# Kernel tuning notes

Hardware: AMD Instinct MI355X
Metric: run time of the kernel (lower is better)

Reference implementation:

```python
import jax, jax.numpy as jnp
import numpy as np

N_NODES = 50000
N_EDGES = 1000000
IN_DIM, HID_DIM, OUT_DIM = 128, 64, 16


def setup_inputs() -> dict:
    key = jax.random.key(0)
    k1, k2, k3, k4 = jax.random.split(key, 4)
    x = jax.random.normal(k1, (N_NODES, IN_DIM), dtype=jnp.float32)
    edge_index = jax.random.randint(k2, (2, N_EDGES), 0, N_NODES, dtype=jnp.int64)
    # Glorot-style scaling for weights, zero bias (PyG GCNConv default init style)
    W1 = jax.random.normal(k3, (IN_DIM, HID_DIM), dtype=jnp.float32) * (1.0 / np.sqrt(IN_DIM))
    b1 = jnp.zeros((HID_DIM,), dtype=jnp.float32)
    W2 = jax.random.normal(k4, (HID_DIM, OUT_DIM), dtype=jnp.float32) * (1.0 / np.sqrt(HID_DIM))
    b2 = jnp.zeros((OUT_DIM,), dtype=jnp.float32)
    return {"x": x, "edge_index": edge_index, "W1": W1, "b1": b1, "W2": W2, "b2": b2}


def gcn_conv(x, src, dst, W, b, num_nodes):
    """PyG GCNConv: add self loops, symmetric deg^{-1/2} normalization,
    linear transform, gather-scale-scatter aggregation, bias."""
    # degree includes self loops (src/dst already augmented by caller)
    deg = jax.ops.segment_sum(jnp.ones_like(dst, dtype=x.dtype), dst, num_segments=num_nodes)
    dinv = jnp.where(deg > 0, deg ** -0.5, 0.0)
    norm = dinv[src] * dinv[dst]            # [E']
    h = x @ W                                # [N, F_out] transform before aggregation
    msg = h[src] * norm[:, None]             # gather + scale
    out = jax.ops.segment_sum(msg, dst, num_segments=num_nodes)  # scatter-add
    return out + b


def reference(x, edge_index, W1, b1, W2, b2):
    n = x.shape[0]
    loops = jnp.arange(n, dtype=edge_index.dtype)
    src = jnp.concatenate([edge_index[0], loops])
    dst = jnp.concatenate([edge_index[1], loops])
    h = gcn_conv(x, src, dst, W1, b1, n)
    h = jax.nn.relu(h)
    out = gcn_conv(h, src, dst, W2, b2, n)
    return out
```

## Files before the change

kernel.cpp:

```cpp
#include <hip/hip_runtime.h>

#define IN_DIM 128
#define HID_DIM 64
#define OUT_DIM 16

#define SSHIFT 7
#define SMASK 127
#define CHUNK 4096
#define CBLK 1024
#define KPT (CHUNK / CBLK)
#define CAP 4096

#define G1S 132

#define SW_OFF   0
#define SX_OFF   32768
#define SDV_OFF  66560
#define SMEM_BYTES 67072

static __device__ __forceinline__ unsigned short f2bf(float f) {
    unsigned u = __float_as_uint(f);
    unsigned r = u + 0x7fffu + ((u >> 16) & 1u);
    return (unsigned short)(r >> 16);
}
static __device__ __forceinline__ unsigned packbf2(float a, float b) {
    return (unsigned)f2bf(a) | ((unsigned)f2bf(b) << 16);
}
static __device__ __forceinline__ float bflo(unsigned v) { return __uint_as_float(v << 16); }
static __device__ __forceinline__ float bfhi(unsigned v) { return __uint_as_float(v & 0xffff0000u); }

__global__ __launch_bounds__(CBLK) void passC2(const int* __restrict__ src,
                                               const int* __restrict__ dst,
                                               int* __restrict__ gcnt,
                                               int* __restrict__ eb,
                                               int E, int NS) {
    __shared__ int cnt[512];
    __shared__ int lofs[512];
    __shared__ int bofs[512];
    __shared__ int cur[512];
    __shared__ int srt[CHUNK];
    int t = threadIdx.x;
    if (t < 512) cnt[t] = 0;
    __syncthreads();
    int base = blockIdx.x * CHUNK;
    int dreg[KPT];
    #pragma unroll
    for (int k = 0; k < KPT; ++k) {
        int i = base + k * CBLK + t;
        int d = -1;
        if (i < E) { d = dst[i]; atomicAdd(&cnt[d >> SSHIFT], 1); }
        dreg[k] = d;
    }
    __syncthreads();
    if (t < 512) lofs[t] = cnt[t];
    __syncthreads();
    for (int off = 1; off < 512; off <<= 1) {
        int tmp = 0;
        if (t < 512 && t >= off) tmp = lofs[t - off];
        __syncthreads();
        if (t < 512) lofs[t] += tmp;
        __syncthreads();
    }
    if (t < 512) {
        int c  = cnt[t];
        int lo = lofs[t] - c;
        lofs[t] = lo;
        cur[t]  = lo;
        bofs[t] = (t < NS && c) ? atomicAdd(&gcnt[t], c) : 0;
    }
    __syncthreads();
    #pragma unroll
    for (int k = 0; k < KPT; ++k) {
        int i = base + k * CBLK + t;
        if (i < E) {
            int d = dreg[k];
            int s = d >> SSHIFT;
            int p = atomicAdd(&cur[s], 1);
            srt[p] = src[i] | ((d & SMASK) << 17);
        }
    }
    __syncthreads();
    int wave = t >> 6, lane = t & 63;
    for (int s = wave; s < NS; s += CBLK / 64) {
        int c  = cnt[s];
        int lo = lofs[s];
        size_t gb = (size_t)s * CAP + bofs[s];
        for (int k = lane; k < c; k += 64) eb[gb + k] = srt[lo + k];
    }
}

__global__ __launch_bounds__(256) void passDG(const int* __restrict__ eb,
                                              const int* __restrict__ tot,
                                              const float* __restrict__ x,
                                              const float* __restrict__ W1,
                                              int* __restrict__ csr_src,
                                              int* __restrict__ row_ptr,
                                              float* __restrict__ dinv,
                                              unsigned* __restrict__ h1u,
                                              int N, int E, int NS) {
    __shared__ __align__(16) char smem[SMEM_BYTES];
    int s = blockIdx.x, t = threadIdx.x;

    {
        int* red  = (int*)smem;
        int* deg  = red + 256;
        int* incl = deg + 128;
        int* cur  = incl + 128;
        int* srt  = cur + 128;
        float* sdv = (float*)(smem + SDV_OFF);

        if (t < 128) deg[t] = 0;
        int part = 0;
        for (int k = t; k < s; k += 256) part += tot[k];
        red[t] = part;
        __syncthreads();
        for (int off = 128; off >= 1; off >>= 1) {
            if (t < off) red[t] += red[t + off];
            __syncthreads();
        }
        int b0 = red[0];
        int cnt = tot[s];
        const size_t sbase = (size_t)s * CAP;
        for (int k = t; k < cnt; k += 256) atomicAdd(&deg[eb[sbase + k] >> 17], 1);
        __syncthreads();
        if (t < 128) incl[t] = deg[t];
        __syncthreads();
        for (int off = 1; off < 128; off <<= 1) {
            int tmp = 0;
            if (t < 128 && t >= off) tmp = incl[t - off];
            __syncthreads();
            if (t < 128) incl[t] += tmp;
            __syncthreads();
        }
        if (t < 128) {
            int loff = incl[t] - deg[t];
            cur[t] = loff;
            float dn = rsqrtf((float)(deg[t] + 1));
            sdv[t] = dn;
            int n = (s << SSHIFT) + t;
            if (n < N) {
                row_ptr[n] = b0 + loff;
                dinv[n] = dn;
            }
        }
        if (s == NS - 1 && t == 0) row_ptr[N] = E;
        __syncthreads();
        for (int k = t; k < cnt; k += 256) {
            int v = eb[sbase + k];
            int dl = v >> 17;
            int p = atomicAdd(&cur[dl], 1);
            srt[p] = v & 0x1FFFF;
        }
        __syncthreads();
        for (int k = t; k < cnt; k += 256) csr_src[b0 + k] = srt[k];
    }
    __syncthreads();

    {
        float* sW  = (float*)(smem + SW_OFF);
        float* sx  = (float*)(smem + SX_OFF);
        float* sdv = (float*)(smem + SDV_OFF);

        const float4* W4  = (const float4*)W1;
        float4*       sW4 = (float4*)sW;
        #pragma unroll
        for (int i = 0; i < 8; ++i) sW4[i * 256 + t] = W4[i * 256 + t];

        const float4* x4 = (const float4*)x;
        int og = t & 15, ng = t >> 4;

        for (int st = 0; st < 2; ++st) {
            int node0 = (s << SSHIFT) + st * 64;
            __syncthreads();
            for (int i = t; i < 64 * 32; i += 256) {
                int r = i >> 5, c = i & 31;
                int n = node0 + r; if (n >= N) n = 0;
                *(float4*)(sx + r * G1S + c * 4) = x4[(size_t)n * 32 + c];
            }
            __syncthreads();

            float a00=0.f,a01=0.f,a02=0.f,a03=0.f, a10=0.f,a11=0.f,a12=0.f,a13=0.f,
                  a20=0.f,a21=0.f,a22=0.f,a23=0.f, a30=0.f,a31=0.f,a32=0.f,a33=0.f;
            const float* xr = sx + (ng << 2) * G1S;
            #pragma unroll 4
            for (int k = 0; k < IN_DIM; ++k) {
                float x0 = xr[k];
                float x1 = xr[G1S + k];
                float x2 = xr[2 * G1S + k];
                float x3 = xr[3 * G1S + k];
                float4 wv = ((const float4*)(sW + k * HID_DIM))[og];
                a00 = fmaf(x0, wv.x, a00); a01 = fmaf(x0, wv.y, a01);
                a02 = fmaf(x0, wv.z, a02); a03 = fmaf(x0, wv.w, a03);
                a10 = fmaf(x1, wv.x, a10); a11 = fmaf(x1, wv.y, a11);
                a12 = fmaf(x1, wv.z, a12); a13 = fmaf(x1, wv.w, a13);
                a20 = fmaf(x2, wv.x, a20); a21 = fmaf(x2, wv.y, a21);
                a22 = fmaf(x2, wv.z, a22); a23 = fmaf(x2, wv.w, a23);
                a30 = fmaf(x3, wv.x, a30); a31 = fmaf(x3, wv.y, a31);
                a32 = fmaf(x3, wv.z, a32); a33 = fmaf(x3, wv.w, a33);
            }

            int lb = st * 64 + (ng << 2);
            int nb = (s << SSHIFT) + st * 64 + (ng << 2);
#define G1_STORE(i, c0, c1, c2, c3)                                         \
            {                                                               \
                int n = nb + i;                                             \
                if (n < N) {                                                \
                    float dn = sdv[lb + i];                                 \
                    uint2 pv;                                               \
                    pv.x = packbf2(c0 * dn, c1 * dn);                       \
                    pv.y = packbf2(c2 * dn, c3 * dn);                       \
                    ((uint2*)(h1u + (size_t)n * 32))[og] = pv;              \
                }                                                           \
            }
            G1_STORE(0, a00, a01, a02, a03)
            G1_STORE(1, a10, a11, a12, a13)
            G1_STORE(2, a20, a21, a22, a23)
            G1_STORE(3, a30, a31, a32, a33)
#undef G1_STORE
        }

        if (s == NS - 1 && t < 16) {
            uint2 z; z.x = 0u; z.y = 0u;
            ((uint2*)(h1u + (size_t)N * 32))[t] = z;
        }
    }
}

__global__ __launch_bounds__(256) void agg1_kernel(const unsigned* __restrict__ h1u,
                                                   const int* __restrict__ row_ptr,
                                                   const int* __restrict__ csr_src,
                                                   const float* __restrict__ dinv,
                                                   const float* __restrict__ b1,
                                                   const float* __restrict__ W2,
                                                   unsigned* __restrict__ h2u, int N) {
    __shared__ __align__(16) float sW[OUT_DIM * 68];
    int t = threadIdx.x;
    for (int i = t; i < HID_DIM * OUT_DIM; i += 256) {
        int k = i >> 4, j = i & 15;
        sW[j * 68 + k] = W2[i];
    }
    __syncthreads();

    int lane = t & 63;
    int h  = lane >> 5;
    int l  = lane & 31;
    int es = l >> 3;
    int dg = l & 7;
    int n = blockIdx.x * 8 + ((t >> 6) << 1) + h;
    if (n > N) return;
    if (n == N) {
        if (l < 4) { uint2 z; z.x = 0u; z.y = 0u; ((uint2*)h2u)[(size_t)N * 4 + l] = z; }
        return;
    }

    int e0 = row_ptr[n], e1 = row_ptr[n + 1];
    const uint4* rb = (const uint4*)h1u;
    int sb = h << 5;

    float a0 = 0.f, a1 = 0.f, a2 = 0.f, a3 = 0.f,
          a4 = 0.f, a5 = 0.f, a6 = 0.f, a7 = 0.f;

    for (int base = e0 - 1; base < e1; base += 32) {
        int idx = base + l;
        int sld = N;
        if (idx == e0 - 1) sld = n;
        else if (idx < e1) sld = csr_src[idx];
        int lim = e1 - base;
        if (lim > 32) lim = 32;
        int nr = (lim + 3) >> 2;
        nr = (nr + 1) & ~1;
        for (int r = 0; r < nr; r += 2) {
            int sA = __shfl(sld, sb + ((r + 0) << 2) + es);
            int sB = __shfl(sld, sb + ((r + 1) << 2) + es);
            uint4 vA = rb[(size_t)sA * 8 + dg];
            uint4 vB = rb[(size_t)sB * 8 + dg];
            a0 += bflo(vA.x) + bflo(vB.x);
            a1 += bfhi(vA.x) + bfhi(vB.x);
            a2 += bflo(vA.y) + bflo(vB.y);
            a3 += bfhi(vA.y) + bfhi(vB.y);
            a4 += bflo(vA.z) + bflo(vB.z);
            a5 += bfhi(vA.z) + bfhi(vB.z);
            a6 += bflo(vA.w) + bflo(vB.w);
            a7 += bfhi(vA.w) + bfhi(vB.w);
        }
    }
    #pragma unroll
    for (int m = 8; m <= 16; m <<= 1) {
        a0 += __shfl_xor(a0, m); a1 += __shfl_xor(a1, m);
        a2 += __shfl_xor(a2, m); a3 += __shfl_xor(a3, m);
        a4 += __shfl_xor(a4, m); a5 += __shfl_xor(a5, m);
        a6 += __shfl_xor(a6, m); a7 += __shfl_xor(a7, m);
    }

    float dn = dinv[n];
    float4 bA = ((const float4*)b1)[2 * dg];
    float4 bB = ((const float4*)b1)[2 * dg + 1];
    float r0 = fmaxf(fmaf(dn, a0, bA.x), 0.f);
    float r1 = fmaxf(fmaf(dn, a1, bA.y), 0.f);
    float r2 = fmaxf(fmaf(dn, a2, bA.z), 0.f);
    float r3 = fmaxf(fmaf(dn, a3, bA.w), 0.f);
    float r4 = fmaxf(fmaf(dn, a4, bB.x), 0.f);
    float r5 = fmaxf(fmaf(dn, a5, bB.y), 0.f);
    float r6 = fmaxf(fmaf(dn, a6, bB.z), 0.f);
    float r7 = fmaxf(fmaf(dn, a7, bB.w), 0.f);

    const float* wb = sW + ((es << 2) * 68) + (dg << 3);
    float4 wA, wB2;
    wA = *(const float4*)(wb);        wB2 = *(const float4*)(wb + 4);
    float p0 = r0*wA.x + r1*wA.y + r2*wA.z + r3*wA.w + r4*wB2.x + r5*wB2.y + r6*wB2.z + r7*wB2.w;
    wA = *(const float4*)(wb + 68);   wB2 = *(const float4*)(wb + 72);
    float p1 = r0*wA.x + r1*wA.y + r2*wA.z + r3*wA.w + r4*wB2.x + r5*wB2.y + r6*wB2.z + r7*wB2.w;
    wA = *(const float4*)(wb + 136);  wB2 = *(const float4*)(wb + 140);
    float p2 = r0*wA.x + r1*wA.y + r2*wA.z + r3*wA.w + r4*wB2.x + r5*wB2.y + r6*wB2.z + r7*wB2.w;
    wA = *(const float4*)(wb + 204);  wB2 = *(const float4*)(wb + 208);
    float p3 = r0*wA.x + r1*wA.y + r2*wA.z + r3*wA.w + r4*wB2.x + r5*wB2.y + r6*wB2.z + r7*wB2.w;

    #pragma unroll
    for (int m = 1; m <= 4; m <<= 1) {
        p0 += __shfl_xor(p0, m); p1 += __shfl_xor(p1, m);
        p2 += __shfl_xor(p2, m); p3 += __shfl_xor(p3, m);
    }
    if (dg == 0) {
        uint2 pv;
        pv.x = packbf2(p0 * dn, p1 * dn);
        pv.y = packbf2(p2 * dn, p3 * dn);
        ((uint2*)h2u)[(size_t)n * 4 + es] = pv;
    }
}

__global__ __launch_bounds__(256) void agg2_kernel(const unsigned* __restrict__ h2u,
                                                   const int* __restrict__ row_ptr,
                                                   const int* __restrict__ csr_src,
                                                   const float* __restrict__ dinv,
                                                   const float* __restrict__ b2,
                                                   float* __restrict__ out, int N) {
    int t = threadIdx.x;
    int lane = t & 63;
    int h  = lane >> 4;
    int l  = lane & 15;
    int es = l >> 2;
    int dg = l & 3;
    int n = blockIdx.x * 16 + ((t >> 6) << 2) + h;
    if (n >= N) return;

    int e0 = row_ptr[n], e1 = row_ptr[n + 1];
    const uint2* rb = (const uint2*)h2u;
    int sb = h << 4;

    float a0 = 0.f, a1 = 0.f, a2 = 0.f, a3 = 0.f;

    for (int base = e0 - 1; base < e1; base += 16) {
        int idx = base + l;
        int sld = N;
        if (idx == e0 - 1) sld = n;
        else if (idx < e1) sld = csr_src[idx];
        int lim = e1 - base;
        if (lim > 16) lim = 16;
        int nr = (lim + 3) >> 2;
        nr = (nr + 1) & ~1;
        for (int r = 0; r < nr; r += 2) {
            int sA = __shfl(sld, sb + ((r + 0) << 2) + es);
            int sB = __shfl(sld, sb + ((r + 1) << 2) + es);
            uint2 vA = rb[(size_t)sA * 4 + dg];
            uint2 vB = rb[(size_t)sB * 4 + dg];
            a0 += bflo(vA.x) + bflo(vB.x);
            a1 += bfhi(vA.x) + bfhi(vB.x);
            a2 += bflo(vA.y) + bflo(vB.y);
            a3 += bfhi(vA.y) + bfhi(vB.y);
        }
    }
    #pragma unroll
    for (int m = 4; m <= 8; m <<= 1) {
        a0 += __shfl_xor(a0, m); a1 += __shfl_xor(a1, m);
        a2 += __shfl_xor(a2, m); a3 += __shfl_xor(a3, m);
    }
    if (es == 0) {
        float dn = dinv[n];
        float4 bb = ((const float4*)b2)[dg];
        float4 r;
        r.x = fmaf(dn, a0, bb.x);
        r.y = fmaf(dn, a1, bb.y);
        r.z = fmaf(dn, a2, bb.z);
        r.w = fmaf(dn, a3, bb.w);
        ((float4*)out)[(size_t)n * 4 + dg] = r;
    }
}

extern "C" void kernel_launch(void* const* d_in, const int* in_sizes, int n_in,
                              void* d_out, int out_size, void* d_ws, size_t ws_size,
                              hipStream_t stream) {
    const float* x  = (const float*)d_in[0];
    const int*   ei = (const int*)d_in[1];
    const float* W1 = (const float*)d_in[2];
    const float* b1 = (const float*)d_in[3];
    const float* W2 = (const float*)d_in[4];
    const float* b2 = (const float*)d_in[5];
    float* out = (float*)d_out;

    const int N = in_sizes[0] / IN_DIM;
    const int E = in_sizes[1] / 2;
    const int* src = ei;
    const int* dst = ei + E;

    const int NS  = (N + SMASK) >> SSHIFT;
    const int NSP = NS + 1;
    const int BC  = (E + CHUNK - 1) / CHUNK;

    char* w = (char*)d_ws;
    auto alloc = [&](size_t bytes) -> void* {
        void* p = (void*)w;
        w += (bytes + 255) & ~(size_t)255;
        return p;
    };
    int*      gcnt    = (int*)     alloc((size_t)NSP * 4);
    int*      eb      = (int*)     alloc((size_t)NS * CAP * 4);
    int*      csr_src = (int*)     alloc((size_t)E * 4);
    int*      row_ptr = (int*)     alloc((size_t)(N + 1) * 4);
    float*    dinv    = (float*)   alloc((size_t)N * 4);
    unsigned* h1u     = (unsigned*)alloc((size_t)(N + 1) * 32 * 4);
    unsigned* h2u     = (unsigned*)alloc((size_t)(N + 1) * 8 * 4);

    const int AB1 = (N + 8) / 8;
    const int AB2 = (N + 15) / 16;

    hipMemsetAsync(gcnt, 0, (size_t)NSP * 4, stream);
    passC2<<<BC, CBLK, 0, stream>>>(src, dst, gcnt, eb, E, NS);
    passDG<<<NS, 256, 0, stream>>>(eb, gcnt, x, W1, csr_src, row_ptr, dinv, h1u, N, E, NS);
    agg1_kernel<<<AB1, 256, 0, stream>>>(h1u, row_ptr, csr_src, dinv, b1, W2, h2u, N);
    agg2_kernel<<<AB2, 256, 0, stream>>>(h2u, row_ptr, csr_src, dinv, b2, out, N);
}
```

Baseline: 156.0 us.

## Split layer-1 aggregation into two feature halves to shrink gather working set

The bf16 hidden features are stored as two separate 32-feature halves instead of one 64-feature row. Layer-1 aggregation runs as two launches, one per half. The first launch stores partial layer-2 projections in an fp32 buffer, and the second adds its own partial and writes h2. The goal is to make each random-gather pass touch a working set small enough to stay in L2 cache. The cost is reading the CSR indices twice, an extra launch, and the partial-sum buffer traffic.

```diff
diff --git a/kernel.cpp b/kernel.cpp
--- a/kernel.cpp
+++ b/kernel.cpp
@@ -96,7 +96,8 @@
                                               int* __restrict__ csr_src,
                                               int* __restrict__ row_ptr,
                                               float* __restrict__ dinv,
-                                              unsigned* __restrict__ h1u,
+                                              unsigned* __restrict__ h1lo,
+                                              unsigned* __restrict__ h1hi,
                                               int N, int E, int NS) {
     __shared__ __align__(16) char smem[SMEM_BYTES];
     int s = blockIdx.x, t = threadIdx.x;
@@ -201,6 +202,8 @@
 
             int lb = st * 64 + (ng << 2);
             int nb = (s << SSHIFT) + st * 64 + (ng << 2);
+            unsigned* hb = (og < 8) ? h1lo : h1hi;
+            int ogl = og & 7;
 #define G1_STORE(i, c0, c1, c2, c3)                                         \
             {                                                               \
                 int n = nb + i;                                             \
@@ -209,7 +212,7 @@
                     uint2 pv;                                               \
                     pv.x = packbf2(c0 * dn, c1 * dn);                       \
                     pv.y = packbf2(c2 * dn, c3 * dn);                       \
-                    ((uint2*)(h1u + (size_t)n * 32))[og] = pv;              \
+                    ((uint2*)(hb + (size_t)n * 16))[ogl] = pv;              \
                 }                                                           \
             }
             G1_STORE(0, a00, a01, a02, a03)
@@ -221,23 +224,26 @@
 
         if (s == NS - 1 && t < 16) {
             uint2 z; z.x = 0u; z.y = 0u;
-            ((uint2*)(h1u + (size_t)N * 32))[t] = z;
-        }
-    }
-}
-
-__global__ __launch_bounds__(256) void agg1_kernel(const unsigned* __restrict__ h1u,
-                                                   const int* __restrict__ row_ptr,
-                                                   const int* __restrict__ csr_src,
-                                                   const float* __restrict__ dinv,
-                                                   const float* __restrict__ b1,
-                                                   const float* __restrict__ W2,
-                                                   unsigned* __restrict__ h2u, int N) {
-    __shared__ __align__(16) float sW[OUT_DIM * 68];
+            if (t < 8) ((uint2*)(h1lo + (size_t)N * 16))[t] = z;
+            else       ((uint2*)(h1hi + (size_t)N * 16))[t - 8] = z;
+        }
+    }
+}
+
+__global__ __launch_bounds__(256) void agg1h_kernel(const unsigned* __restrict__ h1h,
+                                                    const int* __restrict__ row_ptr,
+                                                    const int* __restrict__ csr_src,
+                                                    const float* __restrict__ dinv,
+                                                    const float* __restrict__ b1,
+                                                    const float* __restrict__ W2,
+                                                    float* __restrict__ pbuf,
+                                                    unsigned* __restrict__ h2u,
+                                                    int N, int H) {
+    __shared__ __align__(16) float sW[OUT_DIM * 36];
     int t = threadIdx.x;
-    for (int i = t; i < HID_DIM * OUT_DIM; i += 256) {
+    for (int i = t; i < 32 * OUT_DIM; i += 256) {
         int k = i >> 4, j = i & 15;
-        sW[j * 68 + k] = W2[i];
+        sW[j * 36 + k] = W2[(H * 32 + k) * OUT_DIM + j];
     }
     __syncthreads();
 
@@ -249,16 +255,16 @@
     int n = blockIdx.x * 8 + ((t >> 6) << 1) + h;
     if (n > N) return;
     if (n == N) {
-        if (l < 4) { uint2 z; z.x = 0u; z.y = 0u; ((uint2*)h2u)[(size_t)N * 4 + l] = z; }
+        if (H == 1 && l < 4) { uint2 z; z.x = 0u; z.y = 0u;
+                               ((uint2*)h2u)[(size_t)N * 4 + l] = z; }
         return;
     }
 
     int e0 = row_ptr[n], e1 = row_ptr[n + 1];
-    const uint4* rb = (const uint4*)h1u;
+    const uint2* rb = (const uint2*)h1h;
     int sb = h << 5;
 
-    float a0 = 0.f, a1 = 0.f, a2 = 0.f, a3 = 0.f,
-          a4 = 0.f, a5 = 0.f, a6 = 0.f, a7 = 0.f;
+    float a0 = 0.f, a1 = 0.f, a2 = 0.f, a3 = 0.f;
 
     for (int base = e0 - 1; base < e1; base += 32) {
         int idx = base + l;
@@ -272,48 +278,36 @@
         for (int r = 0; r < nr; r += 2) {
             int sA = __shfl(sld, sb + ((r + 0) << 2) + es);
             int sB = __shfl(sld, sb + ((r + 1) << 2) + es);
-            uint4 vA = rb[(size_t)sA * 8 + dg];
-            uint4 vB = rb[(size_t)sB * 8 + dg];
+            uint2 vA = rb[(size_t)sA * 8 + dg];
+            uint2 vB = rb[(size_t)sB * 8 + dg];
             a0 += bflo(vA.x) + bflo(vB.x);
             a1 += bfhi(vA.x) + bfhi(vB.x);
             a2 += bflo(vA.y) + bflo(vB.y);
             a3 += bfhi(vA.y) + bfhi(vB.y);
-            a4 += bflo(vA.z) + bflo(vB.z);
-            a5 += bfhi(vA.z) + bfhi(vB.z);
-            a6 += bflo(vA.w) + bflo(vB.w);
-            a7 += bfhi(vA.w) + bfhi(vB.w);
         }
     }
     #pragma unroll
     for (int m = 8; m <= 16; m <<= 1) {
         a0 += __shfl_xor(a0, m); a1 += __shfl_xor(a1, m);
         a2 += __shfl_xor(a2, m); a3 += __shfl_xor(a3, m);
-        a4 += __shfl_xor(a4, m); a5 += __shfl_xor(a5, m);
-        a6 += __shfl_xor(a6, m); a7 += __shfl_xor(a7, m);
     }
 
     float dn = dinv[n];
-    float4 bA = ((const float4*)b1)[2 * dg];
-    float4 bB = ((const float4*)b1)[2 * dg + 1];
-    float r0 = fmaxf(fmaf(dn, a0, bA.x), 0.f);
-    float r1 = fmaxf(fmaf(dn, a1, bA.y), 0.f);
-    float r2 = fmaxf(fmaf(dn, a2, bA.z), 0.f);
-    float r3 = fmaxf(fmaf(dn, a3, bA.w), 0.f);
-    float r4 = fmaxf(fmaf(dn, a4, bB.x), 0.f);
-    float r5 = fmaxf(fmaf(dn, a5, bB.y), 0.f);
-    float r6 = fmaxf(fmaf(dn, a6, bB.z), 0.f);
-    float r7 = fmaxf(fmaf(dn, a7, bB.w), 0.f);
-
-    const float* wb = sW + ((es << 2) * 68) + (dg << 3);
-    float4 wA, wB2;
-    wA = *(const float4*)(wb);        wB2 = *(const float4*)(wb + 4);
-    float p0 = r0*wA.x + r1*wA.y + r2*wA.z + r3*wA.w + r4*wB2.x + r5*wB2.y + r6*wB2.z + r7*wB2.w;
-    wA = *(const float4*)(wb + 68);   wB2 = *(const float4*)(wb + 72);
-    float p1 = r0*wA.x + r1*wA.y + r2*wA.z + r3*wA.w + r4*wB2.x + r5*wB2.y + r6*wB2.z + r7*wB2.w;
-    wA = *(const float4*)(wb + 136);  wB2 = *(const float4*)(wb + 140);
-    float p2 = r0*wA.x + r1*wA.y + r2*wA.z + r3*wA.w + r4*wB2.x + r5*wB2.y + r6*wB2.z + r7*wB2.w;
-    wA = *(const float4*)(wb + 204);  wB2 = *(const float4*)(wb + 208);
-    float p3 = r0*wA.x + r1*wA.y + r2*wA.z + r3*wA.w + r4*wB2.x + r5*wB2.y + r6*wB2.z + r7*wB2.w;
+    float4 bb = ((const float4*)b1)[(H << 3) + dg];
+    float r0 = fmaxf(fmaf(dn, a0, bb.x), 0.f);
+    float r1 = fmaxf(fmaf(dn, a1, bb.y), 0.f);
+    float r2 = fmaxf(fmaf(dn, a2, bb.z), 0.f);
+    float r3 = fmaxf(fmaf(dn, a3, bb.w), 0.f);
+
+    const float* wb = sW + ((es << 2) * 36) + (dg << 2);
+    float4 w0 = *(const float4*)(wb);
+    float4 w1 = *(const float4*)(wb + 36);
+    float4 w2v = *(const float4*)(wb + 72);
+    float4 w3 = *(const float4*)(wb + 108);
+    float p0 = r0*w0.x + r1*w0.y + r2*w0.z + r3*w0.w;
+    float p1 = r0*w1.x + r1*w1.y + r2*w1.z + r3*w1.w;
+    float p2 = r0*w2v.x + r1*w2v.y + r2*w2v.z + r3*w2v.w;
+    float p3 = r0*w3.x + r1*w3.y + r2*w3.z + r3*w3.w;
 
     #pragma unroll
     for (int m = 1; m <= 4; m <<= 1) {
@@ -321,10 +315,16 @@
         p2 += __shfl_xor(p2, m); p3 += __shfl_xor(p3, m);
     }
     if (dg == 0) {
-        uint2 pv;
-        pv.x = packbf2(p0 * dn, p1 * dn);
-        pv.y = packbf2(p2 * dn, p3 * dn);
-        ((uint2*)h2u)[(size_t)n * 4 + es] = pv;
+        if (H == 0) {
+            float4 pv; pv.x = p0; pv.y = p1; pv.z = p2; pv.w = p3;
+            ((float4*)pbuf)[(size_t)n * 4 + es] = pv;
+        } else {
+            float4 pl = ((const float4*)pbuf)[(size_t)n * 4 + es];
+            uint2 pv;
+            pv.x = packbf2((p0 + pl.x) * dn, (p1 + pl.y) * dn);
+            pv.y = packbf2((p2 + pl.z) * dn, (p3 + pl.w) * dn);
+            ((uint2*)h2u)[(size_t)n * 4 + es] = pv;
+        }
     }
 }
 
@@ -417,7 +417,9 @@
     int*      csr_src = (int*)     alloc((size_t)E * 4);
     int*      row_ptr = (int*)     alloc((size_t)(N + 1) * 4);
     float*    dinv    = (float*)   alloc((size_t)N * 4);
-    unsigned* h1u     = (unsigned*)alloc((size_t)(N + 1) * 32 * 4);
+    unsigned* h1lo    = (unsigned*)alloc((size_t)(N + 1) * 16 * 4);
+    unsigned* h1hi    = (unsigned*)alloc((size_t)(N + 1) * 16 * 4);
+    float*    pbuf    = (float*)   alloc((size_t)N * 16 * 4);
     unsigned* h2u     = (unsigned*)alloc((size_t)(N + 1) * 8 * 4);
 
     const int AB1 = (N + 8) / 8;
@@ -425,7 +427,11 @@
 
     hipMemsetAsync(gcnt, 0, (size_t)NSP * 4, stream);
     passC2<<<BC, CBLK, 0, stream>>>(src, dst, gcnt, eb, E, NS);
-    passDG<<<NS, 256, 0, stream>>>(eb, gcnt, x, W1, csr_src, row_ptr, dinv, h1u, N, E, NS);
-    agg1_kernel<<<AB1, 256, 0, stream>>>(h1u, row_ptr, csr_src, dinv, b1, W2, h2u, N);
+    passDG<<<NS, 256, 0, stream>>>(eb, gcnt, x, W1, csr_src, row_ptr, dinv,
+                                   h1lo, h1hi, N, E, NS);
+    agg1h_kernel<<<AB1, 256, 0, stream>>>(h1lo, row_ptr, csr_src, dinv, b1, W2,
+                                          pbuf, h2u, N, 0);
+    agg1h_kernel<<<AB1, 256, 0, stream>>>(h1hi, row_ptr, csr_src, dinv, b1, W2,
+                                          pbuf, h2u, N, 1);
     agg2_kernel<<<AB2, 256, 0, stream>>>(h2u, row_ptr, csr_src, dinv, b2, out, N);
 }
```

Result: slower. 165.9 us (+6.3%).
